# Kernel tuning notes

Measured on AMD Instinct MI355X. Metric: run time of the kernel, lower is better.

The kernel has to match this reference:

```python
import jax, jax.numpy as jnp
import numpy as np

EMBED_DIM = 1024
HEAD_DIM = 64


def setup_inputs() -> dict:
    key = jax.random.key(0)
    k1, k2, k3, k4 = jax.random.split(key, 4)
    B, T = 4, 4096
    x = jax.random.normal(k1, (B, T, EMBED_DIM), dtype=jnp.float32)
    # nn.Linear(EMBED_DIM, head_dim, bias=False): store as (EMBED_DIM, head_dim)
    s = (1.0 / np.sqrt(EMBED_DIM)).astype(np.float32)
    Wk = jax.random.uniform(k2, (EMBED_DIM, HEAD_DIM), jnp.float32, -s, s)
    Wq = jax.random.uniform(k3, (EMBED_DIM, HEAD_DIM), jnp.float32, -s, s)
    Wv = jax.random.uniform(k4, (EMBED_DIM, HEAD_DIM), jnp.float32, -s, s)
    return {"x": x, "Wq": Wq, "Wk": Wk, "Wv": Wv}


def reference(x, Wq, Wk, Wv):
    B, T, E = x.shape
    q = jnp.einsum('bte,ed->btd', x, Wq)  # (B,T,D)
    k = jnp.einsum('bte,ed->btd', x, Wk)
    v = jnp.einsum('bte,ed->btd', x, Wv)
    # NOTE: original scales by EMBED_DIM**-0.5 (x.size(-1)), not head_dim**-0.5
    scale = jnp.asarray(E, x.dtype) ** -0.5
    scores = jnp.einsum('bqd,bkd->bqk', q, k) * scale  # (B,T,T)
    causal = jnp.tril(jnp.ones((T, T), dtype=bool))
    scores = jnp.where(causal, scores, jnp.asarray(-jnp.inf, scores.dtype))
    attn = jax.nn.softmax(scores, axis=-1)
    # dropout is identity at inference (deterministic baseline)
    out = jnp.einsum('bqk,bkd->bqd', attn, v)  # (B,T,D)
    return out
```

## Files before the change

### kernel.cpp

```cpp
#include <hip/hip_runtime.h>
#include <hip/hip_bf16.h>
#include <stdint.h>

#define BATCH 4
#define SEQ   4096
#define EMB   1024
#define HD    64

typedef __bf16 bf16x8 __attribute__((ext_vector_type(8)));
typedef float  f32x4  __attribute__((ext_vector_type(4)));
typedef unsigned short u16;

#define QSCALE 0.04508422002777948f

__device__ __forceinline__ u16 f2bf(float f) {
    union { __bf16 h; u16 u; } c; c.h = (__bf16)f; return c.u;
}
__device__ __forceinline__ float bf2f(u16 h) {
    union { uint32_t u; float f; } cv; cv.u = ((uint32_t)h) << 16;
    return cv.f;
}
__device__ __forceinline__ void gld16(const void* g, void* l) {
    __builtin_amdgcn_global_load_lds(
        (const __attribute__((address_space(1))) void*)g,
        (__attribute__((address_space(3))) void*)l, 16, 0, 0);
}

__global__ __launch_bounds__(256) void wt_kernel(
        const float* __restrict__ Wq, const float* __restrict__ Wk,
        const float* __restrict__ Wv, u16* __restrict__ Wt) {
    int idx = blockIdx.x * 256 + threadIdx.x;
    int i = idx >> 16;
    int r = idx & 65535;
    int n = r >> 10;
    int k = r & 1023;
    const float* W = (i == 0) ? Wq : (i == 1) ? Wk : Wv;
    Wt[idx] = f2bf(W[k * HD + n]);
}

__global__ __launch_bounds__(256) void qkv_kernel(
        const float* __restrict__ x, const u16* __restrict__ Wt,
        u16* __restrict__ Qw, u16* __restrict__ Kw, u16* __restrict__ Vt) {
    __shared__ float xs[2][2048];
    __shared__ u16   wsb[2][12288];

    const int t    = threadIdx.x;
    const int wave = t >> 6;
    const int lane = t & 63;
    const int m16  = lane & 15;
    const int quad = lane >> 4;
    const int rh   = wave & 1;
    const int ch   = wave >> 1;
    const int R0   = blockIdx.x * 32;

    #define ISSUE(buf_, kt_) do {                                              \
        const int r4_ = lane >> 4, c16_ = lane & 15;                           \
        _Pragma("unroll")                                                      \
        for (int j_ = 0; j_ < 2; ++j_) {                                       \
            const int ii_  = wave + (j_ << 2);                                 \
            const int row_ = (ii_ << 2) + r4_;                      \
            const int kc_  = c16_ ^ (row_ & 15);                               \
            gld16(x + (size_t)(R0 + row_) * EMB + ((kt_) << 6) + (kc_ << 2),   \
                  &xs[buf_][ii_ << 8]);                                        \
        }                                                                      \
        const int r8_ = lane >> 3, c8_ = lane & 7;                             \
        _Pragma("unroll")                                                      \
        for (int j_ = 0; j_ < 6; ++j_) {                                       \
            const int rb_ = (wave * 6 + j_) << 3;                  \
            const int kw_ = c8_ ^ r8_;                                         \
            gld16(Wt + (size_t)(rb_ + r8_) * 1024 + ((kt_) << 6) + (kw_ << 3), \
                  &wsb[buf_][(wave * 6 + j_) << 9]);                           \
        }                                                                      \
    } while (0)

    f32x4 acc[6];
#pragma unroll
    for (int a = 0; a < 6; ++a) acc[a] = (f32x4){0.f, 0.f, 0.f, 0.f};

    const int row_x = rh * 16 + m16;
    ISSUE(0, 0);

    for (int kt = 0; kt < 16; ++kt) {
        const int buf = kt & 1;
        __syncthreads();
        if (kt < 15) ISSUE(buf ^ 1, kt + 1);

#pragma unroll
        for (int ks2 = 0; ks2 < 2; ++ks2) {
            const int c0 = (ks2 << 3) + (quad << 1);
            const float4 a0 = *(const float4*)&xs[buf][(row_x << 6) + ((c0 ^ m16) << 2)];
            const float4 a1 = *(const float4*)&xs[buf][(row_x << 6) + (((c0 + 1) ^ m16) << 2)];
            union { bf16x8 v; __bf16 e[8]; } af;
            af.e[0] = (__bf16)a0.x; af.e[1] = (__bf16)a0.y;
            af.e[2] = (__bf16)a0.z; af.e[3] = (__bf16)a0.w;
            af.e[4] = (__bf16)a1.x; af.e[5] = (__bf16)a1.y;
            af.e[6] = (__bf16)a1.z; af.e[7] = (__bf16)a1.w;
#pragma unroll
            for (int i = 0; i < 6; ++i) {
                const int tt   = ch * 6 + i;
                const int rowW = (tt << 4) + m16;
                const bf16x8 bf = *(const bf16x8*)&wsb[buf][
                        (rowW << 6) + ((((ks2 << 2) + quad) ^ (m16 & 7)) << 3)];
                acc[i] = __builtin_amdgcn_mfma_f32_16x16x32_bf16(af.v, bf, acc[i], 0, 0, 0);
            }
        }
    }
    #undef ISSUE

    const int rowbase = R0 + rh * 16 + (quad << 2);
    const int bidx = rowbase >> 12;
    const int t0   = rowbase & 4095;
#pragma unroll
    for (int i = 0; i < 6; ++i) {
        const int tt  = ch * 6 + i;
        const int w3  = tt >> 2;
        const int col = ((tt & 3) << 4) + m16;
        if (w3 == 0) {
#pragma unroll
            for (int reg = 0; reg < 4; ++reg)
                Qw[(size_t)(rowbase + reg) * HD + col] = f2bf(acc[i][reg] * QSCALE);
        } else if (w3 == 1) {
#pragma unroll
            for (int reg = 0; reg < 4; ++reg)
                Kw[(size_t)(rowbase + reg) * HD + col] = f2bf(acc[i][reg]);
        } else {
            union { ushort4 vv; __bf16 e[4]; } o;
            o.e[0] = (__bf16)acc[i][0]; o.e[1] = (__bf16)acc[i][1];
            o.e[2] = (__bf16)acc[i][2]; o.e[3] = (__bf16)acc[i][3];
            *(ushort4*)(Vt + (size_t)((bidx << 6) + col) * SEQ + t0) = o.vv;
        }
    }
}

__global__ __launch_bounds__(256, 4) void attn_part_kernel(
        const u16* __restrict__ Qw, const u16* __restrict__ Kw,
        const u16* __restrict__ Vt, u16* __restrict__ Opart,
        float* __restrict__ Mp, float* __restrict__ Lp) {
    __shared__ u16 kv[2][2][4096];
    __shared__ u16 ldsP[4][1024];

    const int pid = blockIdx.x;
    const int r   = pid >> 8;
    const int i   = pid & 255;
    const int b   = i & 3;
    const int h   = i >> 2;
    const int qt  = h ^ (int)((0x1f203f00u >> (r * 8)) & 63u);
    const int c   = r;
    const int p_out = (((b << 6) + qt) << 2) + c;

    const int wave = threadIdx.x >> 6;
    const int lane = threadIdx.x & 63;
    const int m16  = lane & 15;
    const int quad = lane >> 4;

    #define ISSUE_KV(buf_, jt_) do {                                           \
        const int r8_ = lane >> 3, c8_ = lane & 7;                             \
        const int kc_ = c8_ ^ r8_;                                             \
        _Pragma("unroll")                                                      \
        for (int j_ = 0; j_ < 2; ++j_) {                                       \
            const int row_ = ((wave * 2 + j_) << 3) + r8_;          \
            gld16(Kw + ((size_t)(b * SEQ + ((jt_) << 6) + row_) << 6) + (kc_ << 3), \
                  &kv[buf_][0][(wave * 2 + j_) << 9]);                         \
            gld16(Vt + (size_t)((b << 6) + row_) * SEQ + ((jt_) << 6) + (kc_ << 3), \
                  &kv[buf_][1][(wave * 2 + j_) << 9]);                         \
        }                                                                      \
    } while (0)

    const int qrow = (qt << 6) + (wave << 4) + m16;
    const u16* qbase = Qw + ((size_t)(b * SEQ + qrow) << 6);
    const bf16x8 qf0 = *(const bf16x8*)(qbase + (quad << 3));
    const bf16x8 qf1 = *(const bf16x8*)(qbase + 32 + (quad << 3));

    f32x4 acc[4];
#pragma unroll
    for (int dt = 0; dt < 4; ++dt) acc[dt] = (f32x4){0.f, 0.f, 0.f, 0.f};
    float m_i = -3.0e38f;
    float l_i = 0.f;

    u16* ldsW = &ldsP[wave][0];
    const int xs0 = (quad ^ (m16 & 7)) << 3;
    const int xs1 = (((quad + 4)) ^ (m16 & 7)) << 3;
    const int psw = m16 & 7;

    if (c <= qt) ISSUE_KV(0, c);

    int buf = 0;
    for (int jt = c; jt <= qt; jt += 4) {
        __syncthreads();
        if (jt + 4 <= qt) ISSUE_KV(buf ^ 1, jt + 4);

        f32x4 s[4];
#pragma unroll
        for (int mt = 0; mt < 4; ++mt) {
            const int base = ((mt << 4) + m16) << 6;
            bf16x8 k0 = *(const bf16x8*)&kv[buf][0][base + xs0];
            bf16x8 k1 = *(const bf16x8*)&kv[buf][0][base + xs1];
            s[mt] = (f32x4){0.f, 0.f, 0.f, 0.f};
            s[mt] = __builtin_amdgcn_mfma_f32_16x16x32_bf16(k0, qf0, s[mt], 0, 0, 0);
            s[mt] = __builtin_amdgcn_mfma_f32_16x16x32_bf16(k1, qf1, s[mt], 0, 0, 0);
        }

        if (jt == qt) {
            const int q_in = (wave << 4) + m16;
#pragma unroll
            for (int mt = 0; mt < 4; ++mt) {
                const int k_in = (mt << 4) + (quad << 2);
#pragma unroll
                for (int reg = 0; reg < 4; ++reg)
                    if (k_in + reg > q_in) s[mt][reg] = -3.0e38f;
            }
        }

        float tm = fmaxf(fmaxf(s[0][0], s[0][1]), fmaxf(s[0][2], s[0][3]));
#pragma unroll
        for (int mt = 1; mt < 4; ++mt)
            tm = fmaxf(tm, fmaxf(fmaxf(s[mt][0], s[mt][1]), fmaxf(s[mt][2], s[mt][3])));
        tm = fmaxf(tm, __shfl_xor(tm, 16));
        tm = fmaxf(tm, __shfl_xor(tm, 32));

        if (__any(tm > m_i + 8.0f)) {
            const float mnew  = fmaxf(m_i, tm);
            const float alpha = __builtin_amdgcn_exp2f(m_i - mnew);
            m_i = mnew;
            l_i *= alpha;
#pragma unroll
            for (int dt = 0; dt < 4; ++dt)
#pragma unroll
                for (int reg = 0; reg < 4; ++reg) acc[dt][reg] *= alpha;
        }

        float psum = 0.f;
#pragma unroll
        for (int mt = 0; mt < 4; ++mt) {
            const float p0 = __builtin_amdgcn_exp2f(s[mt][0] - m_i);
            const float p1 = __builtin_amdgcn_exp2f(s[mt][1] - m_i);
            const float p2 = __builtin_amdgcn_exp2f(s[mt][2] - m_i);
            const float p3 = __builtin_amdgcn_exp2f(s[mt][3] - m_i);
            psum += (p0 + p1) + (p2 + p3);
            union { ushort4 pv; __bf16 e[4]; } u;
            u.e[0] = (__bf16)p0; u.e[1] = (__bf16)p1;
            u.e[2] = (__bf16)p2; u.e[3] = (__bf16)p3;
            const int c8 = ((mt << 1) + (quad >> 1)) ^ psw;
            *(ushort4*)(ldsW + (m16 << 6) + (c8 << 3) + ((quad & 1) << 2)) = u.pv;
        }
        l_i += psum;

        const bf16x8 p0 = *(const bf16x8*)(ldsW + (m16 << 6) + ((quad ^ psw) << 3));
        const bf16x8 p1 = *(const bf16x8*)(ldsW + (m16 << 6) + (((quad + 4) ^ psw) << 3));
#pragma unroll
        for (int dt = 0; dt < 4; ++dt) {
            const int base = ((dt << 4) + m16) << 6;
            bf16x8 v0 = *(const bf16x8*)&kv[buf][1][base + xs0];
            bf16x8 v1 = *(const bf16x8*)&kv[buf][1][base + xs1];
            acc[dt] = __builtin_amdgcn_mfma_f32_16x16x32_bf16(v0, p0, acc[dt], 0, 0, 0);
            acc[dt] = __builtin_amdgcn_mfma_f32_16x16x32_bf16(v1, p1, acc[dt], 0, 0, 0);
        }
        buf ^= 1;
    }
    #undef ISSUE_KV

    float l = l_i;
    l += __shfl_xor(l, 16);
    l += __shfl_xor(l, 32);

    u16* ob = Opart + (size_t)p_out * 4096;
    const int qin = (wave << 4) + m16;
#pragma unroll
    for (int dt = 0; dt < 4; ++dt) {
        union { ushort4 vv; __bf16 e[4]; } o;
        o.e[0] = (__bf16)acc[dt][0]; o.e[1] = (__bf16)acc[dt][1];
        o.e[2] = (__bf16)acc[dt][2]; o.e[3] = (__bf16)acc[dt][3];
        *(ushort4*)(ob + qin * 64 + (dt << 4) + (quad << 2)) = o.vv;
    }
    if (quad == 0) {
        Mp[p_out * 64 + qin] = m_i;
        Lp[p_out * 64 + qin] = l;
    }
}

__global__ __launch_bounds__(256) void combine_kernel(
        const u16* __restrict__ Opart, const float* __restrict__ Mp,
        const float* __restrict__ Lp, float* __restrict__ out) {
    __shared__ float sm[4][16];
    __shared__ float sl[4][16];
    const int bq = blockIdx.x >> 2;
    const int rq = blockIdx.x & 3;
    const int pidbase = bq << 2;
    const int t = threadIdx.x;
    if (t < 64) {
        const int cc = t >> 4, rr = t & 15;
        sm[cc][rr] = Mp[(pidbase + cc) * 64 + rq * 16 + rr];
        sl[cc][rr] = Lp[(pidbase + cc) * 64 + rq * 16 + rr];
    }
    __syncthreads();

    const int row_l = t >> 4;
    const int c4    = (t & 15) << 2;
    const int row   = rq * 16 + row_l;

    const float M = fmaxf(fmaxf(sm[0][row_l], sm[1][row_l]),
                          fmaxf(sm[2][row_l], sm[3][row_l]));
    float n0 = 0.f, n1 = 0.f, n2 = 0.f, n3 = 0.f, den = 0.f;
#pragma unroll
    for (int cc = 0; cc < 4; ++cc) {
        const float w = __builtin_amdgcn_exp2f(sm[cc][row_l] - M);
        den += w * sl[cc][row_l];
        const ushort4 op = *(const ushort4*)&Opart[
                (size_t)(pidbase + cc) * 4096 + row * 64 + c4];
        n0 += w * bf2f(op.x); n1 += w * bf2f(op.y);
        n2 += w * bf2f(op.z); n3 += w * bf2f(op.w);
    }
    const float rd = 1.0f / den;
    float4 o; o.x = n0 * rd; o.y = n1 * rd; o.z = n2 * rd; o.w = n3 * rd;
    *(float4*)&out[((size_t)bq << 12) + (row << 6) + c4] = o;
}

extern "C" void kernel_launch(void* const* d_in, const int* in_sizes, int n_in,
                              void* d_out, int out_size, void* d_ws, size_t ws_size,
                              hipStream_t stream) {
    const float* x  = (const float*)d_in[0];
    const float* Wq = (const float*)d_in[1];
    const float* Wk = (const float*)d_in[2];
    const float* Wv = (const float*)d_in[3];
    float* out = (float*)d_out;

    char* ws = (char*)d_ws;
    u16* Qw    = (u16*)(ws);
    u16* Kw    = (u16*)(ws + (2u << 20));
    u16* Vt    = (u16*)(ws + (4u << 20));
    u16* Wt    = (u16*)(ws + (6u << 20));
    u16* Opart = (u16*)(ws + (13u << 19));
    float* Mp  = (float*)(ws + (29u << 19));
    float* Lp  = (float*)(ws + (59u << 18));

    wt_kernel<<<768, 256, 0, stream>>>(Wq, Wk, Wv, Wt);
    qkv_kernel<<<512, 256, 0, stream>>>(x, Wt, Qw, Kw, Vt);
    attn_part_kernel<<<1024, 256, 0, stream>>>(Qw, Kw, Vt, Opart, Mp, Lp);
    combine_kernel<<<1024, 256, 0, stream>>>(Opart, Mp, Lp, out);
}
```

Measured before the change: 144.4 us.

## Switch attention to 32x32x16 MFMA with 128-row query tiles and register P reuse

The attention kernel now uses 32x32x16 bf16 MFMA on 128-row query tiles, with 8 key-split partitions per tile instead of 4. The probability matrix is repacked in registers through permlane32 swaps rather than a round trip through LDS, so the LDS P buffer goes away. Partial outputs are stored as fp32 in a transposed layout, and the combine kernel is rewritten to merge 8 partials per row. The aim is fewer LDS round trips and better MFMA efficiency, paid for with more accumulator registers, larger fp32 partial traffic, and extra causal-skip branches that may leave work unevenly spread across blocks.

New measurement: 143.4 us. Within noise of the previous version (-0.7%).

```diff
diff --git a/kernel.cpp b/kernel.cpp
--- a/kernel.cpp
+++ b/kernel.cpp
@@ -9,6 +9,8 @@
 
 typedef __bf16 bf16x8 __attribute__((ext_vector_type(8)));
 typedef float  f32x4  __attribute__((ext_vector_type(4)));
+typedef float  f32x16 __attribute__((ext_vector_type(16)));
+typedef unsigned u32x2v __attribute__((ext_vector_type(2)));
 typedef unsigned short u16;
 
 #define QSCALE 0.04508422002777948f
@@ -16,14 +18,27 @@
 __device__ __forceinline__ u16 f2bf(float f) {
     union { __bf16 h; u16 u; } c; c.h = (__bf16)f; return c.u;
 }
-__device__ __forceinline__ float bf2f(u16 h) {
-    union { uint32_t u; float f; } cv; cv.u = ((uint32_t)h) << 16;
-    return cv.f;
+__device__ __forceinline__ unsigned pk2(float lo, float hi) {
+    union { __bf16 e[2]; unsigned u; } c;
+    c.e[0] = (__bf16)lo; c.e[1] = (__bf16)hi; return c.u;
 }
 __device__ __forceinline__ void gld16(const void* g, void* l) {
     __builtin_amdgcn_global_load_lds(
         (const __attribute__((address_space(1))) void*)g,
         (__attribute__((address_space(3))) void*)l, 16, 0, 0);
+}
+__device__ __forceinline__ void halfswap(unsigned &a, unsigned &b) {
+#if __has_builtin(__builtin_amdgcn_permlane32_swap)
+    u32x2v r = __builtin_amdgcn_permlane32_swap(a, b, false, false);
+    a = r.x; b = r.y;
+#else
+    const unsigned pa = (unsigned)__shfl_xor((int)a, 32);
+    const unsigned pb = (unsigned)__shfl_xor((int)b, 32);
+    const bool hi = (threadIdx.x & 32) != 0;
+    const unsigned na = hi ? pb : a;
+    const unsigned nb = hi ? b : pa;
+    a = na; b = nb;
+#endif
 }
 
 __global__ __launch_bounds__(256) void wt_kernel(
@@ -134,24 +149,23 @@
 
 __global__ __launch_bounds__(256, 4) void attn_part_kernel(
         const u16* __restrict__ Qw, const u16* __restrict__ Kw,
-        const u16* __restrict__ Vt, u16* __restrict__ Opart,
+        const u16* __restrict__ Vt, float* __restrict__ Opart,
         float* __restrict__ Mp, float* __restrict__ Lp) {
     __shared__ u16 kv[2][2][4096];
-    __shared__ u16 ldsP[4][1024];
 
     const int pid = blockIdx.x;
-    const int r   = pid >> 8;
-    const int i   = pid & 255;
+    const int c   = pid >> 7;
+    const int i   = pid & 127;
     const int b   = i & 3;
-    const int h   = i >> 2;
-    const int qt  = h ^ (int)((0x1f203f00u >> (r * 8)) & 63u);
-    const int c   = r;
-    const int p_out = (((b << 6) + qt) << 2) + c;
+    const int hq  = i >> 2;
+    const int qt  = hq ^ (int)((0x071817080F101F00ULL >> (c * 8)) & 31u);
+    const int part = (((b << 5) + qt) << 3) + c;
+    const int jmax = 2 * qt + 1;
 
     const int wave = threadIdx.x >> 6;
     const int lane = threadIdx.x & 63;
-    const int m16  = lane & 15;
-    const int quad = lane >> 4;
+    const int l31  = lane & 31;
+    const int h    = lane >> 5;
 
     #define ISSUE_KV(buf_, jt_) do {                                           \
         const int r8_ = lane >> 3, c8_ = lane & 7;                             \
@@ -166,153 +180,179 @@
         }                                                                      \
     } while (0)
 
-    const int qrow = (qt << 6) + (wave << 4) + m16;
-    const u16* qbase = Qw + ((size_t)(b * SEQ + qrow) << 6);
-    const bf16x8 qf0 = *(const bf16x8*)(qbase + (quad << 3));
-    const bf16x8 qf1 = *(const bf16x8*)(qbase + 32 + (quad << 3));
-
-    f32x4 acc[4];
-#pragma unroll
-    for (int dt = 0; dt < 4; ++dt) acc[dt] = (f32x4){0.f, 0.f, 0.f, 0.f};
-    float m_i = -3.0e38f;
-    float l_i = 0.f;
-
-    u16* ldsW = &ldsP[wave][0];
-    const int xs0 = (quad ^ (m16 & 7)) << 3;
-    const int xs1 = (((quad + 4)) ^ (m16 & 7)) << 3;
-    const int psw = m16 & 7;
-
-    if (c <= qt) ISSUE_KV(0, c);
+    const int qg = (qt << 7) + (wave << 5) + l31;
+    const u16* qbase = Qw + ((size_t)(b * SEQ + qg) << 6);
+    bf16x8 qf[4];
+#pragma unroll
+    for (int s = 0; s < 4; ++s)
+        qf[s] = *(const bf16x8*)(qbase + (s << 4) + (h << 3));
+
+    f32x16 o[2];
+#pragma unroll
+    for (int dt = 0; dt < 2; ++dt)
+#pragma unroll
+        for (int k = 0; k < 16; ++k) o[dt][k] = 0.f;
+    float m_i = -3.0e38f, l_i = 0.f;
+    const int qmin_w = (qt << 7) + (wave << 5);
+
+    if (c <= jmax) ISSUE_KV(0, c);
 
     int buf = 0;
-    for (int jt = c; jt <= qt; jt += 4) {
+    for (int jt = c; jt <= jmax; jt += 8) {
         __syncthreads();
-        if (jt + 4 <= qt) ISSUE_KV(buf ^ 1, jt + 4);
-
-        f32x4 s[4];
-#pragma unroll
-        for (int mt = 0; mt < 4; ++mt) {
-            const int base = ((mt << 4) + m16) << 6;
-            bf16x8 k0 = *(const bf16x8*)&kv[buf][0][base + xs0];
-            bf16x8 k1 = *(const bf16x8*)&kv[buf][0][base + xs1];
-            s[mt] = (f32x4){0.f, 0.f, 0.f, 0.f};
-            s[mt] = __builtin_amdgcn_mfma_f32_16x16x32_bf16(k0, qf0, s[mt], 0, 0, 0);
-            s[mt] = __builtin_amdgcn_mfma_f32_16x16x32_bf16(k1, qf1, s[mt], 0, 0, 0);
-        }
-
-        if (jt == qt) {
-            const int q_in = (wave << 4) + m16;
-#pragma unroll
-            for (int mt = 0; mt < 4; ++mt) {
-                const int k_in = (mt << 4) + (quad << 2);
-#pragma unroll
-                for (int reg = 0; reg < 4; ++reg)
-                    if (k_in + reg > q_in) s[mt][reg] = -3.0e38f;
-            }
-        }
-
-        float tm = fmaxf(fmaxf(s[0][0], s[0][1]), fmaxf(s[0][2], s[0][3]));
-#pragma unroll
-        for (int mt = 1; mt < 4; ++mt)
-            tm = fmaxf(tm, fmaxf(fmaxf(s[mt][0], s[mt][1]), fmaxf(s[mt][2], s[mt][3])));
-        tm = fmaxf(tm, __shfl_xor(tm, 16));
-        tm = fmaxf(tm, __shfl_xor(tm, 32));
-
-        if (__any(tm > m_i + 8.0f)) {
-            const float mnew  = fmaxf(m_i, tm);
-            const float alpha = __builtin_amdgcn_exp2f(m_i - mnew);
-            m_i = mnew;
-            l_i *= alpha;
-#pragma unroll
-            for (int dt = 0; dt < 4; ++dt)
-#pragma unroll
-                for (int reg = 0; reg < 4; ++reg) acc[dt][reg] *= alpha;
-        }
-
-        float psum = 0.f;
-#pragma unroll
-        for (int mt = 0; mt < 4; ++mt) {
-            const float p0 = __builtin_amdgcn_exp2f(s[mt][0] - m_i);
-            const float p1 = __builtin_amdgcn_exp2f(s[mt][1] - m_i);
-            const float p2 = __builtin_amdgcn_exp2f(s[mt][2] - m_i);
-            const float p3 = __builtin_amdgcn_exp2f(s[mt][3] - m_i);
-            psum += (p0 + p1) + (p2 + p3);
-            union { ushort4 pv; __bf16 e[4]; } u;
-            u.e[0] = (__bf16)p0; u.e[1] = (__bf16)p1;
-            u.e[2] = (__bf16)p2; u.e[3] = (__bf16)p3;
-            const int c8 = ((mt << 1) + (quad >> 1)) ^ psw;
-            *(ushort4*)(ldsW + (m16 << 6) + (c8 << 3) + ((quad & 1) << 2)) = u.pv;
-        }
-        l_i += psum;
-
-        const bf16x8 p0 = *(const bf16x8*)(ldsW + (m16 << 6) + ((quad ^ psw) << 3));
-        const bf16x8 p1 = *(const bf16x8*)(ldsW + (m16 << 6) + (((quad + 4) ^ psw) << 3));
-#pragma unroll
-        for (int dt = 0; dt < 4; ++dt) {
-            const int base = ((dt << 4) + m16) << 6;
-            bf16x8 v0 = *(const bf16x8*)&kv[buf][1][base + xs0];
-            bf16x8 v1 = *(const bf16x8*)&kv[buf][1][base + xs1];
-            acc[dt] = __builtin_amdgcn_mfma_f32_16x16x32_bf16(v0, p0, acc[dt], 0, 0, 0);
-            acc[dt] = __builtin_amdgcn_mfma_f32_16x16x32_bf16(v1, p1, acc[dt], 0, 0, 0);
+        if (jt + 8 <= jmax) ISSUE_KV(buf ^ 1, jt + 8);
+
+        if ((jt << 6) <= qmin_w + 31) {
+            f32x16 s2[2];
+#pragma unroll
+            for (int mt = 0; mt < 2; ++mt) {
+                f32x16 sa;
+#pragma unroll
+                for (int k = 0; k < 16; ++k) sa[k] = 0.f;
+                const int row = (mt << 5) + l31;
+                const int rb  = row << 6;
+                const int rx  = row & 7;
+#pragma unroll
+                for (int s = 0; s < 4; ++s) {
+                    const bf16x8 kf = *(const bf16x8*)&kv[buf][0][
+                            rb + ((((s << 1) + h) ^ rx) << 3)];
+                    sa = __builtin_amdgcn_mfma_f32_32x32x16_bf16(kf, qf[s], sa, 0, 0, 0);
+                }
+                s2[mt] = sa;
+            }
+
+            if ((jt << 6) + 63 > qmin_w) {
+#pragma unroll
+                for (int mt = 0; mt < 2; ++mt)
+#pragma unroll
+                for (int reg = 0; reg < 16; ++reg) {
+                    const int kg = (jt << 6) + (mt << 5) +
+                                   (reg & 3) + ((reg >> 2) << 3) + (h << 2);
+                    if (kg > qg) s2[mt][reg] = -3.0e38f;
+                }
+            }
+
+            float tm = s2[0][0];
+#pragma unroll
+            for (int mt = 0; mt < 2; ++mt)
+#pragma unroll
+            for (int reg = 0; reg < 16; ++reg) tm = fmaxf(tm, s2[mt][reg]);
+            tm = fmaxf(tm, __shfl_xor(tm, 32));
+
+            if (__any(tm > m_i + 8.0f)) {
+                const float mnew = fmaxf(m_i, tm);
+                const float al = __builtin_amdgcn_exp2f(m_i - mnew);
+                m_i = mnew; l_i *= al;
+#pragma unroll
+                for (int dt = 0; dt < 2; ++dt)
+#pragma unroll
+                for (int k = 0; k < 16; ++k) o[dt][k] *= al;
+            }
+
+            float ps = 0.f;
+#pragma unroll
+            for (int mt = 0; mt < 2; ++mt)
+#pragma unroll
+            for (int reg = 0; reg < 16; ++reg) {
+                const float p = __builtin_amdgcn_exp2f(s2[mt][reg] - m_i);
+                s2[mt][reg] = p; ps += p;
+            }
+            l_i += ps;
+
+            union F { unsigned d[4]; bf16x8 v; } pf[4];
+#pragma unroll
+            for (int mt = 0; mt < 2; ++mt) {
+                unsigned A0 = pk2(s2[mt][0],  s2[mt][1]);
+                unsigned B0 = pk2(s2[mt][4],  s2[mt][5]);
+                unsigned C0 = pk2(s2[mt][2],  s2[mt][3]);
+                unsigned D0 = pk2(s2[mt][6],  s2[mt][7]);
+                halfswap(A0, B0); halfswap(C0, D0);
+                pf[2*mt].d[0] = A0; pf[2*mt].d[1] = C0;
+                pf[2*mt].d[2] = B0; pf[2*mt].d[3] = D0;
+                unsigned A1 = pk2(s2[mt][8],  s2[mt][9]);
+                unsigned B1 = pk2(s2[mt][12], s2[mt][13]);
+                unsigned C1 = pk2(s2[mt][10], s2[mt][11]);
+                unsigned D1 = pk2(s2[mt][14], s2[mt][15]);
+                halfswap(A1, B1); halfswap(C1, D1);
+                pf[2*mt+1].d[0] = A1; pf[2*mt+1].d[1] = C1;
+                pf[2*mt+1].d[2] = B1; pf[2*mt+1].d[3] = D1;
+            }
+
+#pragma unroll
+            for (int dt = 0; dt < 2; ++dt) {
+                const int row = (dt << 5) + l31;
+                const int rb  = row << 6;
+                const int rx  = row & 7;
+                f32x16 oa = o[dt];
+#pragma unroll
+                for (int s = 0; s < 4; ++s) {
+                    const bf16x8 vf = *(const bf16x8*)&kv[buf][1][
+                            rb + ((((s << 1) + h) ^ rx) << 3)];
+                    oa = __builtin_amdgcn_mfma_f32_32x32x16_bf16(vf, pf[s].v, oa, 0, 0, 0);
+                }
+                o[dt] = oa;
+            }
         }
         buf ^= 1;
     }
     #undef ISSUE_KV
 
-    float l = l_i;
-    l += __shfl_xor(l, 16);
-    l += __shfl_xor(l, 32);
-
-    u16* ob = Opart + (size_t)p_out * 4096;
-    const int qin = (wave << 4) + m16;
-#pragma unroll
-    for (int dt = 0; dt < 4; ++dt) {
-        union { ushort4 vv; __bf16 e[4]; } o;
-        o.e[0] = (__bf16)acc[dt][0]; o.e[1] = (__bf16)acc[dt][1];
-        o.e[2] = (__bf16)acc[dt][2]; o.e[3] = (__bf16)acc[dt][3];
-        *(ushort4*)(ob + qin * 64 + (dt << 4) + (quad << 2)) = o.vv;
-    }
-    if (quad == 0) {
-        Mp[p_out * 64 + qin] = m_i;
-        Lp[p_out * 64 + qin] = l;
+    const float l2 = l_i + __shfl_xor(l_i, 32);
+
+    float* ob = Opart + ((size_t)part << 13) + (wave << 5) + l31;
+#pragma unroll
+    for (int dt = 0; dt < 2; ++dt)
+#pragma unroll
+    for (int reg = 0; reg < 16; ++reg) {
+        const int d = (dt << 5) + (reg & 3) + ((reg >> 2) << 3) + (h << 2);
+        ob[d << 7] = o[dt][reg];
+    }
+    if (lane < 32) {
+        Mp[part * 128 + (wave << 5) + l31] = m_i;
+        Lp[part * 128 + (wave << 5) + l31] = l2;
     }
 }
 
 __global__ __launch_bounds__(256) void combine_kernel(
-        const u16* __restrict__ Opart, const float* __restrict__ Mp,
+        const float* __restrict__ Opart, const float* __restrict__ Mp,
         const float* __restrict__ Lp, float* __restrict__ out) {
-    __shared__ float sm[4][16];
-    __shared__ float sl[4][16];
-    const int bq = blockIdx.x >> 2;
-    const int rq = blockIdx.x & 3;
-    const int pidbase = bq << 2;
-    const int t = threadIdx.x;
-    if (t < 64) {
-        const int cc = t >> 4, rr = t & 15;
-        sm[cc][rr] = Mp[(pidbase + cc) * 64 + rq * 16 + rr];
-        sl[cc][rr] = Lp[(pidbase + cc) * 64 + rq * 16 + rr];
-    }
-    __syncthreads();
-
-    const int row_l = t >> 4;
-    const int c4    = (t & 15) << 2;
-    const int row   = rq * 16 + row_l;
-
-    const float M = fmaxf(fmaxf(sm[0][row_l], sm[1][row_l]),
-                          fmaxf(sm[2][row_l], sm[3][row_l]));
-    float n0 = 0.f, n1 = 0.f, n2 = 0.f, n3 = 0.f, den = 0.f;
-#pragma unroll
-    for (int cc = 0; cc < 4; ++cc) {
-        const float w = __builtin_amdgcn_exp2f(sm[cc][row_l] - M);
-        den += w * sl[cc][row_l];
-        const ushort4 op = *(const ushort4*)&Opart[
-                (size_t)(pidbase + cc) * 4096 + row * 64 + c4];
-        n0 += w * bf2f(op.x); n1 += w * bf2f(op.y);
-        n2 += w * bf2f(op.z); n3 += w * bf2f(op.w);
+    const int gb = blockIdx.x;
+    const int bq = gb >> 1;
+    const int qh = gb & 1;
+    const int t  = threadIdx.x;
+    const int ql = (qh << 6) + (t & 63);
+    const int d0 = (t >> 6) << 4;
+    const int pb = bq << 3;
+
+    float mv[8];
+    float M = -3.0e38f;
+#pragma unroll
+    for (int cc = 0; cc < 8; ++cc) {
+        mv[cc] = Mp[(pb + cc) * 128 + ql];
+        M = fmaxf(M, mv[cc]);
+    }
+    float o16[16];
+#pragma unroll
+    for (int k = 0; k < 16; ++k) o16[k] = 0.f;
+    float den = 0.f;
+#pragma unroll
+    for (int cc = 0; cc < 8; ++cc) {
+        const float w = __builtin_amdgcn_exp2f(mv[cc] - M);
+        den += w * Lp[(pb + cc) * 128 + ql];
+        const float* op = Opart + ((size_t)(pb + cc) << 13) + ql;
+#pragma unroll
+        for (int k = 0; k < 16; ++k)
+            o16[k] = fmaf(w, op[(d0 + k) << 7], o16[k]);
     }
     const float rd = 1.0f / den;
-    float4 o; o.x = n0 * rd; o.y = n1 * rd; o.z = n2 * rd; o.w = n3 * rd;
-    *(float4*)&out[((size_t)bq << 12) + (row << 6) + c4] = o;
+    float* orow = out + (((size_t)bq << 7) + ql) * 64 + d0;
+#pragma unroll
+    for (int j = 0; j < 4; ++j) {
+        float4 v;
+        v.x = o16[4*j]     * rd; v.y = o16[4*j + 1] * rd;
+        v.z = o16[4*j + 2] * rd; v.w = o16[4*j + 3] * rd;
+        *(float4*)(orow + 4*j) = v;
+    }
 }
 
 extern "C" void kernel_launch(void* const* d_in, const int* in_sizes, int n_in,
@@ -325,16 +365,16 @@
     float* out = (float*)d_out;
 
     char* ws = (char*)d_ws;
-    u16* Qw    = (u16*)(ws);
-    u16* Kw    = (u16*)(ws + (2u << 20));
-    u16* Vt    = (u16*)(ws + (4u << 20));
-    u16* Wt    = (u16*)(ws + (6u << 20));
-    u16* Opart = (u16*)(ws + (13u << 19));
-    float* Mp  = (float*)(ws + (29u << 19));
-    float* Lp  = (float*)(ws + (59u << 18));
+    u16* Qw     = (u16*)(ws);
+    u16* Kw     = (u16*)(ws + (2u << 20));
+    u16* Vt     = (u16*)(ws + (4u << 20));
+    u16* Wt     = (u16*)(ws + (6u << 20));
+    float* Opart = (float*)(ws + (8u << 20));
+    float* Mp   = (float*)(ws + (40u << 20));
+    float* Lp   = (float*)(ws + (40u << 20) + (512u << 10));
 
     wt_kernel<<<768, 256, 0, stream>>>(Wq, Wk, Wv, Wt);
     qkv_kernel<<<512, 256, 0, stream>>>(x, Wt, Qw, Kw, Vt);
     attn_part_kernel<<<1024, 256, 0, stream>>>(Qw, Kw, Vt, Opart, Mp, Lp);
-    combine_kernel<<<1024, 256, 0, stream>>>(Opart, Mp, Lp, out);
-}
+    combine_kernel<<<256, 256, 0, stream>>>(Opart, Mp, Lp, out);
+}
```
